# Kernel tuning notes

Hardware: AMD Instinct MI355X
Metric: run time of the kernel (lower is better)

## Reference

```python
import jax, jax.numpy as jnp
import numpy as np

N, E, G = 50000, 200000, 64
F, H, C = 1536, 1024, 80
FUSE = 1024


def setup_inputs() -> dict:
    key = jax.random.key(0)
    ks = jax.random.split(key, 12)
    def lin(k, fan_in, shape):
        return jax.random.normal(k, shape, dtype=jnp.float32) / np.sqrt(fan_in)
    return {
        "global_x": jax.random.normal(ks[0], (G, F), dtype=jnp.float32),
        "x": jax.random.normal(ks[1], (N, F), dtype=jnp.float32),
        "edge_index": jax.random.randint(ks[2], (2, E), 0, N),
        "batch": jnp.sort(jax.random.randint(ks[3], (N,), 0, G)),
        "W1": lin(ks[4], F, (F, H)), "b1": jnp.zeros((H,), jnp.float32),
        "W2": lin(ks[5], H, (H, H)), "b2": jnp.zeros((H,), jnp.float32),
        "fw1": lin(ks[6], F + H, (F + H, FUSE)), "fb1": jnp.zeros((FUSE,), jnp.float32),
        "fw2": lin(ks[7], FUSE, (FUSE, C)), "fb2": jnp.zeros((C,), jnp.float32),
    }


def _gcn_conv(x, src, dst, norm, W, b):
    # x' = D^-1/2 (A+I) D^-1/2 (x W) + b   (PyG GCNConv, add_self_loops=True)
    h = x @ W                                   # [N, H]
    msg = h[src] * norm[:, None]                # [E+N, H] gather + scale
    out = jax.ops.segment_sum(msg, dst, num_segments=N)  # scatter-add
    return out + b


def reference(global_x, x, edge_index, batch, W1, b1, W2, b2, fw1, fb1, fw2, fb2):
    loops = jnp.arange(N)
    src = jnp.concatenate([edge_index[0], loops])  # add self-loops
    dst = jnp.concatenate([edge_index[1], loops])
    deg = jax.ops.segment_sum(jnp.ones(E + N, jnp.float32), dst, num_segments=N)
    dis = jnp.where(deg > 0, jax.lax.rsqrt(jnp.maximum(deg, 1.0)), 0.0)
    norm = dis[src] * dis[dst]                  # symmetric normalization

    h = jax.nn.relu(_gcn_conv(x, src, dst, norm, W1, b1))
    h = jax.nn.relu(_gcn_conv(h, src, dst, norm, W2, b2))

    counts = jax.ops.segment_sum(jnp.ones(N, jnp.float32), batch, num_segments=G)
    pooled = jax.ops.segment_sum(h, batch, num_segments=G) / jnp.maximum(counts, 1.0)[:, None]

    combined = jnp.concatenate([global_x, pooled], axis=1)  # [G, F+H]
    hid = jax.nn.relu(combined @ fw1 + fb1)     # dropout is identity in eval
    return hid @ fw2 + fb2                      # [G, C]
```

## Files before the change

### kernel.cpp

```cpp
#include <hip/hip_runtime.h>
#include <stdint.h>

#define N_NODES 50000
#define N_EDGES 200000
#define N_GRAPH 64
#define F_IN    1536
#define H_DIM   1024
#define C_OUT   80
#define FUSE_D  1024
#define POOL_CHUNK 128
#define MLP1_KC 320
#define SCAN_B  49

typedef unsigned short u16;
typedef short s16x8 __attribute__((ext_vector_type(8)));
typedef float f32x4 __attribute__((ext_vector_type(4)));
typedef unsigned short u16x4 __attribute__((ext_vector_type(4)));
typedef unsigned short u16x8 __attribute__((ext_vector_type(8)));

__device__ __forceinline__ float bf2f(u16 u) {
    union { unsigned int i; float f; } v; v.i = ((unsigned int)u) << 16; return v.f;
}
__device__ __forceinline__ u16 f2bf(float f) {
    union { float f; unsigned int i; } v; v.f = f;
    unsigned int x = v.i;
    unsigned int r = (x + 0x7fffu + ((x >> 16) & 1u)) >> 16;
    return (u16)r;
}

__device__ __forceinline__ void load_lds16(const void* g, void* l) {
    __builtin_amdgcn_global_load_lds(
        (const __attribute__((address_space(1))) void*)g,
        (__attribute__((address_space(3))) void*)l, 16, 0, 0);
}

__global__ void k_deg(const int* __restrict__ dst, int* cnt) {
    int e = blockIdx.x * blockDim.x + threadIdx.x;
    if (e < N_EDGES) atomicAdd(&cnt[dst[e]], 1);
}

__global__ void k_cg(const int* __restrict__ batch, int* cG) {
    int i = blockIdx.x * blockDim.x + threadIdx.x;
    if (i < N_NODES) atomicAdd(&cG[batch[i]], 1);
}

__global__ __launch_bounds__(1024) void k_scan_a(const int* __restrict__ cnt, int* __restrict__ bsum) {
    __shared__ int lds[1024];
    int t = threadIdx.x;
    int i = blockIdx.x * 1024 + t;
    lds[t] = (i < N_NODES) ? cnt[i] : 0;
    __syncthreads();
    for (int off = 512; off > 0; off >>= 1) {
        if (t < off) lds[t] += lds[t + off];
        __syncthreads();
    }
    if (t == 0) bsum[blockIdx.x] = lds[0];
}

__global__ __launch_bounds__(64) void k_scan_b(const int* __restrict__ bsum,
                                               int* __restrict__ boff, int* __restrict__ rowptr) {
    int t = threadIdx.x;
    int v = (t < SCAN_B) ? bsum[t] : 0;
    for (int off = 1; off < 64; off <<= 1) {
        int u = __shfl_up(v, off);
        if (t >= off) v += u;
    }
    if (t < SCAN_B) boff[t] = v - bsum[t];
    if (t == SCAN_B - 1) rowptr[N_NODES] = v;
}

__global__ __launch_bounds__(1024) void k_scan_c(const int* __restrict__ cnt, const int* __restrict__ boff,
                                                 int* __restrict__ rowptr, float* __restrict__ dis) {
    __shared__ int lds[1024];
    int t = threadIdx.x;
    int i = blockIdx.x * 1024 + t;
    int c = (i < N_NODES) ? cnt[i] : 0;
    lds[t] = c;
    __syncthreads();
    for (int off = 1; off < 1024; off <<= 1) {
        int u = (t >= off) ? lds[t - off] : 0;
        __syncthreads();
        lds[t] += u;
        __syncthreads();
    }
    if (i < N_NODES) {
        rowptr[i] = boff[blockIdx.x] + lds[t] - c;
        dis[i] = rsqrtf((float)(c + 1));
    }
}

__global__ void k_fill(const int* __restrict__ src, const int* __restrict__ dst,
                       const int* __restrict__ rowptr, int* cursor, int* col) {
    int e = blockIdx.x * blockDim.x + threadIdx.x;
    if (e < N_EDGES) {
        int d = dst[e];
        int p = atomicAdd(&cursor[d], 1);
        col[rowptr[d] + p] = src[e];
    }
}

__global__ void k_cvt(const float* __restrict__ in, u16* __restrict__ out, long n) {
    long i = (long)blockIdx.x * blockDim.x + threadIdx.x;
    long stride = (long)gridDim.x * blockDim.x;
    for (long v = i * 4; v < n; v += stride * 4) {
        float4 f = *(const float4*)(in + v);
        u16x4 o = { f2bf(f.x), f2bf(f.y), f2bf(f.z), f2bf(f.w) };
        *(u16x4*)(out + v) = o;
    }
}

__global__ void k_trn(const float* __restrict__ W, u16* __restrict__ Wt, int K, int Nn) {
    __shared__ float tle[32][33];
    int n0 = blockIdx.x * 32, k0 = blockIdx.y * 32;
    int tx = threadIdx.x, ty = threadIdx.y;
    for (int i = ty; i < 32; i += 8)
        tle[i][tx] = W[(size_t)(k0 + i) * Nn + n0 + tx];
    __syncthreads();
    for (int i = ty; i < 32; i += 8)
        Wt[(size_t)(n0 + i) * K + k0 + tx] = f2bf(tle[tx][i]);
}

__global__ __launch_bounds__(512) void gemm_bt(const u16* __restrict__ A,
                                               const u16* __restrict__ Bt,
                                               u16* __restrict__ C,
                                               int M, int Nn, int K) {
    __shared__ __attribute__((aligned(16))) u16 ldsA[2 * 2048 * 8];
    __shared__ __attribute__((aligned(16))) u16 ldsB[2 * 2048 * 8];

    int bid = blockIdx.x;
    int swz = (bid & 7) * 98 + (bid >> 3);
    int bN = swz & 3;
    int bM = swz >> 2;

    int tid = threadIdx.x;
    int lane = tid & 63, wave = tid >> 6;
    int wm = wave >> 2, wn = wave & 3;
    int qd = lane >> 4, lo = lane & 15;

    const u16* ga[4];
    const u16* gb[4];
#pragma unroll
    for (int r = 0; r < 4; ++r) {
        int c = r * 512 + tid;
        int row = c >> 3;
        int kc = (c & 7) ^ (row & 7);
        int gr = bM * 256 + row;
        if (gr > M - 1) gr = M - 1;
        ga[r] = A + (size_t)gr * K + kc * 8;
        gb[r] = Bt + (size_t)(bN * 256 + row) * K + kc * 8;
    }

    auto stage = [&](int buf) {
        int base = buf * 16384;
#pragma unroll
        for (int r = 0; r < 4; ++r) {
            load_lds16(ga[r], &ldsA[base + (r * 512 + tid) * 8]);
            ga[r] += 64;
        }
#pragma unroll
        for (int r = 0; r < 4; ++r) {
            load_lds16(gb[r], &ldsB[base + (r * 512 + tid) * 8]);
            gb[r] += 64;
        }
    };

    const int NKT = K >> 6;
    f32x4 acc[8][4] = {};

    stage(0);
    stage(1);

    for (int kt = 0; kt < NKT; ++kt) {
        int cur = kt & 1;
        if (kt < NKT - 1) {
            asm volatile("s_waitcnt vmcnt(8)" ::: "memory");
        } else {
            asm volatile("s_waitcnt vmcnt(0)" ::: "memory");
        }
        __builtin_amdgcn_s_barrier();

        const u16* lA = ldsA + cur * 16384;
        const u16* lB = ldsB + cur * 16384;
#pragma unroll
        for (int ks = 0; ks < 2; ++ks) {
            s16x8 af[8], bfv[4];
            int soff = (((ks << 2) + qd) ^ (lo & 7)) * 8;
#pragma unroll
            for (int mf = 0; mf < 8; ++mf)
                af[mf] = *(const s16x8*)&lA[(wm * 128 + mf * 16 + lo) * 64 + soff];
#pragma unroll
            for (int nf = 0; nf < 4; ++nf)
                bfv[nf] = *(const s16x8*)&lB[(wn * 64 + nf * 16 + lo) * 64 + soff];
            __builtin_amdgcn_s_setprio(1);
#pragma unroll
            for (int mf = 0; mf < 8; ++mf)
#pragma unroll
                for (int nf = 0; nf < 4; ++nf)
                    acc[mf][nf] = __builtin_amdgcn_mfma_f32_16x16x32_bf16(
                        af[mf], bfv[nf], acc[mf][nf], 0, 0, 0);
            __builtin_amdgcn_s_setprio(0);
            __builtin_amdgcn_s_barrier();
        }
        if (kt + 2 < NKT) stage(cur);
    }

#pragma unroll
    for (int mf = 0; mf < 8; ++mf) {
        int rowb = bM * 256 + wm * 128 + mf * 16 + qd * 4;
#pragma unroll
        for (int nf = 0; nf < 4; ++nf) {
            int colI = bN * 256 + wn * 64 + nf * 16 + lo;
            f32x4 a = acc[mf][nf];
#pragma unroll
            for (int reg = 0; reg < 4; ++reg) {
                int row = rowb + reg;
                if (row < M) C[(size_t)row * Nn + colI] = f2bf(a[reg]);
            }
        }
    }
}

__global__ __launch_bounds__(256) void k_agg(const u16* __restrict__ hin, u16* __restrict__ hout,
                                             const int* __restrict__ rowptr, const int* __restrict__ col,
                                             const float* __restrict__ dis, const float* __restrict__ bias) {
    int w = threadIdx.x >> 6, lane = threadIdx.x & 63;
    int i = blockIdx.x * 4 + w;
    float di = dis[i];
    int beg = rowptr[i], end = rowptr[i + 1];
    const u16* hrow = hin + (size_t)i * H_DIM + lane * 16;
    u16x8 v0 = *(const u16x8*)hrow;
    u16x8 v1 = *(const u16x8*)(hrow + 8);
    float w0 = di * di;
    float acc[16];
#pragma unroll
    for (int j = 0; j < 8; j++) { acc[j] = w0 * bf2f(v0[j]); acc[8 + j] = w0 * bf2f(v1[j]); }
    int e = beg;
    for (; e + 2 <= end; e += 2) {
        int s0 = col[e], s1 = col[e + 1];
        float g0 = di * dis[s0], g1 = di * dis[s1];
        const u16* n0 = hin + (size_t)s0 * H_DIM + lane * 16;
        const u16* n1 = hin + (size_t)s1 * H_DIM + lane * 16;
        u16x8 a0 = *(const u16x8*)n0;
        u16x8 a1 = *(const u16x8*)(n0 + 8);
        u16x8 b0 = *(const u16x8*)n1;
        u16x8 b1 = *(const u16x8*)(n1 + 8);
#pragma unroll
        for (int j = 0; j < 8; j++) {
            acc[j]     += g0 * bf2f(a0[j]) + g1 * bf2f(b0[j]);
            acc[8 + j] += g0 * bf2f(a1[j]) + g1 * bf2f(b1[j]);
        }
    }
    if (e < end) {
        int s = col[e];
        float wgt = di * dis[s];
        const u16* nrow = hin + (size_t)s * H_DIM + lane * 16;
        u16x8 u0 = *(const u16x8*)nrow;
        u16x8 u1 = *(const u16x8*)(nrow + 8);
#pragma unroll
        for (int j = 0; j < 8; j++) { acc[j] += wgt * bf2f(u0[j]); acc[8 + j] += wgt * bf2f(u1[j]); }
    }
    const float* bp = bias + lane * 16;
    u16x8 o0, o1;
#pragma unroll
    for (int j = 0; j < 8; j++) {
        o0[j] = f2bf(fmaxf(acc[j] + bp[j], 0.f));
        o1[j] = f2bf(fmaxf(acc[8 + j] + bp[8 + j], 0.f));
    }
    u16* orow = hout + (size_t)i * H_DIM + lane * 16;
    *(u16x8*)orow = o0;
    *(u16x8*)(orow + 8) = o1;
}

__global__ __launch_bounds__(256) void k_pool(const u16* __restrict__ h, const int* __restrict__ batch,
                                              float* __restrict__ pooled) {
    int t = threadIdx.x;
    int n0 = blockIdx.x * POOL_CHUNK;
    int n1 = min(n0 + POOL_CHUNK, N_NODES);
    float a0 = 0.f, a1 = 0.f, a2 = 0.f, a3 = 0.f;
    int curg = batch[n0];
    for (int n = n0; n < n1; ++n) {
        int g = batch[n];
        if (g != curg) {
            float* p = &pooled[(size_t)curg * H_DIM + t * 4];
            atomicAdd(p + 0, a0); atomicAdd(p + 1, a1);
            atomicAdd(p + 2, a2); atomicAdd(p + 3, a3);
            a0 = a1 = a2 = a3 = 0.f;
            curg = g;
        }
        u16x4 v = *(const u16x4*)&h[(size_t)n * H_DIM + t * 4];
        a0 += bf2f(v[0]); a1 += bf2f(v[1]); a2 += bf2f(v[2]); a3 += bf2f(v[3]);
    }
    float* p = &pooled[(size_t)curg * H_DIM + t * 4];
    atomicAdd(p + 0, a0); atomicAdd(p + 1, a1);
    atomicAdd(p + 2, a2); atomicAdd(p + 3, a3);
}

__global__ __launch_bounds__(256) void k_mlp1(const float* __restrict__ gx, const float* __restrict__ pooled,
                                              const int* __restrict__ cG,
                                              const float* __restrict__ fw1, float* __restrict__ hid) {
    __shared__ float comb[4 * MLP1_KC];
    int gq = blockIdx.x, jq = blockIdx.y, kq = blockIdx.z, t = threadIdx.x;
    int kbeg = kq * MLP1_KC;
    for (int idx = t; idx < 4 * MLP1_KC; idx += 256) {
        int gl = idx / MLP1_KC, kk = idx % MLP1_KC;
        int k = kbeg + kk;
        int g = gq * 4 + gl;
        float v;
        if (k < F_IN) v = gx[(size_t)g * F_IN + k];
        else v = pooled[(size_t)g * H_DIM + (k - F_IN)] / (float)max(cG[g], 1);
        comb[idx] = v;
    }
    __syncthreads();
    int j = jq * 256 + t;
    float a0 = 0, a1 = 0, a2 = 0, a3 = 0;
    for (int kk = 0; kk < MLP1_KC; ++kk) {
        float w = fw1[(size_t)(kbeg + kk) * FUSE_D + j];
        a0 += comb[kk] * w;
        a1 += comb[MLP1_KC + kk] * w;
        a2 += comb[2 * MLP1_KC + kk] * w;
        a3 += comb[3 * MLP1_KC + kk] * w;
    }
    atomicAdd(&hid[(size_t)(gq * 4 + 0) * FUSE_D + j], a0);
    atomicAdd(&hid[(size_t)(gq * 4 + 1) * FUSE_D + j], a1);
    atomicAdd(&hid[(size_t)(gq * 4 + 2) * FUSE_D + j], a2);
    atomicAdd(&hid[(size_t)(gq * 4 + 3) * FUSE_D + j], a3);
}

__global__ __launch_bounds__(128) void k_mlp2(const float* __restrict__ hid, const float* __restrict__ fb1,
                                              const float* __restrict__ fw2,
                                              const float* __restrict__ fb2, float* __restrict__ out) {
    __shared__ float hh[FUSE_D];
    int g = blockIdx.x, t = threadIdx.x;
    for (int idx = t; idx < FUSE_D; idx += 128)
        hh[idx] = fmaxf(hid[(size_t)g * FUSE_D + idx] + fb1[idx], 0.f);
    __syncthreads();
    if (t < C_OUT) {
        float acc = fb2[t];
        for (int k = 0; k < FUSE_D; ++k) acc += hh[k] * fw2[k * C_OUT + t];
        out[g * C_OUT + t] = acc;
    }
}

extern "C" void kernel_launch(void* const* d_in, const int* in_sizes, int n_in,
                              void* d_out, int out_size, void* d_ws, size_t ws_size,
                              hipStream_t stream) {
    (void)in_sizes; (void)n_in; (void)out_size;
    const float* gx    = (const float*)d_in[0];
    const float* x     = (const float*)d_in[1];
    const int*   ei    = (const int*)d_in[2];
    const int*   batch = (const int*)d_in[3];
    const float* W1    = (const float*)d_in[4];
    const float* b1    = (const float*)d_in[5];
    const float* W2    = (const float*)d_in[6];
    const float* b2    = (const float*)d_in[7];
    const float* fw1   = (const float*)d_in[8];
    const float* fb1   = (const float*)d_in[9];
    const float* fw2   = (const float*)d_in[10];
    const float* fb2   = (const float*)d_in[11];
    float* out = (float*)d_out;
    const int* src = ei;
    const int* dst = ei + N_EDGES;

    char* ws = (char*)d_ws;
    size_t off = 0;
    auto alloc = [&](size_t bytes) -> char* {
        char* p = ws + off;
        off += (bytes + 255) & ~(size_t)255;
        return p;
    };
    u16*  xb     = (u16*)alloc((size_t)N_NODES * F_IN * 2);
    u16*  h0b    = (u16*)alloc((size_t)N_NODES * H_DIM * 2);
    u16*  h1b    = (u16*)alloc((size_t)N_NODES * H_DIM * 2);
    u16*  W1T    = (u16*)alloc((size_t)H_DIM * F_IN * 2);
    u16*  W2T    = (u16*)alloc((size_t)H_DIM * H_DIM * 2);
    float* dis    = (float*)alloc((size_t)N_NODES * 4);
    int* rowptr   = (int*)alloc((size_t)(N_NODES + 1) * 4);
    int* col      = (int*)alloc((size_t)N_EDGES * 4);
    int* cnt      = (int*)alloc((size_t)N_NODES * 4);
    int* cursor   = (int*)alloc((size_t)N_NODES * 4);
    int* cG       = (int*)alloc(256);
    float* pooled = (float*)alloc((size_t)N_GRAPH * H_DIM * 4);
    float* hid    = (float*)alloc((size_t)N_GRAPH * FUSE_D * 4);
    u16* h2b = xb;
    u16* h3b = h0b;
    int* bsum = col;
    int* boff = col + 64;
    (void)ws_size;

    size_t zbytes = (size_t)((char*)(hid + N_GRAPH * FUSE_D) - (char*)cnt);
    hipMemsetAsync(cnt, 0, zbytes, stream);

    k_deg<<<(N_EDGES + 255) / 256, 256, 0, stream>>>(dst, cnt);
    k_cg<<<(N_NODES + 255) / 256, 256, 0, stream>>>(batch, cG);
    k_scan_a<<<SCAN_B, 1024, 0, stream>>>(cnt, bsum);
    k_scan_b<<<1, 64, 0, stream>>>(bsum, boff, rowptr);
    k_scan_c<<<SCAN_B, 1024, 0, stream>>>(cnt, boff, rowptr, dis);
    k_fill<<<(N_EDGES + 255) / 256, 256, 0, stream>>>(src, dst, rowptr, cursor, col);

    k_cvt<<<4096, 256, 0, stream>>>(x, xb, (long)N_NODES * F_IN);
    k_trn<<<dim3(H_DIM / 32, F_IN / 32), dim3(32, 8), 0, stream>>>(W1, W1T, F_IN, H_DIM);
    k_trn<<<dim3(H_DIM / 32, H_DIM / 32), dim3(32, 8), 0, stream>>>(W2, W2T, H_DIM, H_DIM);

    const int GEMM_BLOCKS = ((N_NODES + 255) / 256) * (H_DIM / 256);

    gemm_bt<<<GEMM_BLOCKS, 512, 0, stream>>>(xb, W1T, h0b, N_NODES, H_DIM, F_IN);
    k_agg<<<N_NODES / 4, 256, 0, stream>>>(h0b, h1b, rowptr, col, dis, b1);
    gemm_bt<<<GEMM_BLOCKS, 512, 0, stream>>>(h1b, W2T, h2b, N_NODES, H_DIM, H_DIM);
    k_agg<<<N_NODES / 4, 256, 0, stream>>>(h2b, h3b, rowptr, col, dis, b2);

    k_pool<<<(N_NODES + POOL_CHUNK - 1) / POOL_CHUNK, 256, 0, stream>>>(h3b, batch, pooled);
    k_mlp1<<<dim3(N_GRAPH / 4, FUSE_D / 256, 8), 256, 0, stream>>>(gx, pooled, cG, fw1, hid);
    k_mlp2<<<N_GRAPH, 128, 0, stream>>>(hid, fb1, fw2, fb2, out);
}
```

Baseline: 1.500 ms.

## Deepen GEMM LDS pipeline to 4 stages with K-tile 32; widen MLP1 graph batching

The bf16 GEMM now uses a K-tile of 32 instead of 64, with four LDS buffers and three tiles prefetched ahead. The swizzle is adapted to 4-chunk rows, and one of the two barriers per iteration is removed. The aim is to hide global-load latency better while keeping the same LDS footprint. The cost is twice as many loop iterations, each doing half the MFMA work, so per-iteration overhead is relatively larger. MLP1 also handles 8 graphs per block instead of 4, which halves the number of fw1 weight reads.

```diff
diff --git a/kernel.cpp b/kernel.cpp
--- a/kernel.cpp
+++ b/kernel.cpp
@@ -10,6 +10,7 @@
 #define FUSE_D  1024
 #define POOL_CHUNK 128
 #define MLP1_KC 320
+#define MLP1_G  8
 #define SCAN_B  49
 
 typedef unsigned short u16;
@@ -124,8 +125,8 @@
                                                const u16* __restrict__ Bt,
                                                u16* __restrict__ C,
                                                int M, int Nn, int K) {
-    __shared__ __attribute__((aligned(16))) u16 ldsA[2 * 2048 * 8];
-    __shared__ __attribute__((aligned(16))) u16 ldsB[2 * 2048 * 8];
+    __shared__ __attribute__((aligned(16))) u16 ldsA[4 * 8192];
+    __shared__ __attribute__((aligned(16))) u16 ldsB[4 * 8192];
 
     int bid = blockIdx.x;
     int swz = (bid & 7) * 98 + (bid >> 3);
@@ -137,13 +138,13 @@
     int wm = wave >> 2, wn = wave & 3;
     int qd = lane >> 4, lo = lane & 15;
 
-    const u16* ga[4];
-    const u16* gb[4];
-#pragma unroll
-    for (int r = 0; r < 4; ++r) {
+    const u16* ga[2];
+    const u16* gb[2];
+#pragma unroll
+    for (int r = 0; r < 2; ++r) {
         int c = r * 512 + tid;
-        int row = c >> 3;
-        int kc = (c & 7) ^ (row & 7);
+        int row = c >> 2;
+        int kc = (c & 3) ^ ((row >> 1) & 3);
         int gr = bM * 256 + row;
         if (gr > M - 1) gr = M - 1;
         ga[r] = A + (size_t)gr * K + kc * 8;
@@ -151,57 +152,58 @@
     }
 
     auto stage = [&](int buf) {
-        int base = buf * 16384;
-#pragma unroll
-        for (int r = 0; r < 4; ++r) {
+        int base = buf * 8192;
+#pragma unroll
+        for (int r = 0; r < 2; ++r)
             load_lds16(ga[r], &ldsA[base + (r * 512 + tid) * 8]);
-            ga[r] += 64;
-        }
-#pragma unroll
-        for (int r = 0; r < 4; ++r) {
+#pragma unroll
+        for (int r = 0; r < 2; ++r)
             load_lds16(gb[r], &ldsB[base + (r * 512 + tid) * 8]);
-            gb[r] += 64;
-        }
+#pragma unroll
+        for (int r = 0; r < 2; ++r) { ga[r] += 32; gb[r] += 32; }
     };
 
-    const int NKT = K >> 6;
+    const int NKT = K >> 5;
     f32x4 acc[8][4] = {};
 
     stage(0);
     stage(1);
+    stage(2);
+
+    const int sl = (qd ^ ((lo >> 1) & 3)) * 8;
 
     for (int kt = 0; kt < NKT; ++kt) {
-        int cur = kt & 1;
-        if (kt < NKT - 1) {
+        int cur = kt & 3;
+        if (kt < NKT - 2) {
             asm volatile("s_waitcnt vmcnt(8)" ::: "memory");
+        } else if (kt == NKT - 2) {
+            asm volatile("s_waitcnt vmcnt(4)" ::: "memory");
         } else {
             asm volatile("s_waitcnt vmcnt(0)" ::: "memory");
         }
         __builtin_amdgcn_s_barrier();
 
-        const u16* lA = ldsA + cur * 16384;
-        const u16* lB = ldsB + cur * 16384;
-#pragma unroll
-        for (int ks = 0; ks < 2; ++ks) {
-            s16x8 af[8], bfv[4];
-            int soff = (((ks << 2) + qd) ^ (lo & 7)) * 8;
-#pragma unroll
-            for (int mf = 0; mf < 8; ++mf)
-                af[mf] = *(const s16x8*)&lA[(wm * 128 + mf * 16 + lo) * 64 + soff];
+        const u16* lA = ldsA + cur * 8192;
+        const u16* lB = ldsB + cur * 8192;
+        s16x8 af[8], bv[4];
+#pragma unroll
+        for (int mf = 0; mf < 8; ++mf)
+            af[mf] = *(const s16x8*)&lA[(wm * 128 + mf * 16 + lo) * 32 + sl];
+#pragma unroll
+        for (int nf = 0; nf < 4; ++nf)
+            bv[nf] = *(const s16x8*)&lB[(wn * 64 + nf * 16 + lo) * 32 + sl];
+        asm volatile("s_waitcnt lgkmcnt(0)" ::: "memory");
+        __builtin_amdgcn_sched_barrier(0);
+        __builtin_amdgcn_s_setprio(1);
+#pragma unroll
+        for (int mf = 0; mf < 8; ++mf)
 #pragma unroll
             for (int nf = 0; nf < 4; ++nf)
-                bfv[nf] = *(const s16x8*)&lB[(wn * 64 + nf * 16 + lo) * 64 + soff];
-            __builtin_amdgcn_s_setprio(1);
-#pragma unroll
-            for (int mf = 0; mf < 8; ++mf)
-#pragma unroll
-                for (int nf = 0; nf < 4; ++nf)
-                    acc[mf][nf] = __builtin_amdgcn_mfma_f32_16x16x32_bf16(
-                        af[mf], bfv[nf], acc[mf][nf], 0, 0, 0);
-            __builtin_amdgcn_s_setprio(0);
-            __builtin_amdgcn_s_barrier();
-        }
-        if (kt + 2 < NKT) stage(cur);
+                acc[mf][nf] = __builtin_amdgcn_mfma_f32_16x16x32_bf16(
+                    af[mf], bv[nf], acc[mf][nf], 0, 0, 0);
+        __builtin_amdgcn_s_setprio(0);
+
+        if (kt + 3 < NKT) stage((kt + 3) & 3);
     }
 
 #pragma unroll
@@ -298,13 +300,13 @@
 __global__ __launch_bounds__(256) void k_mlp1(const float* __restrict__ gx, const float* __restrict__ pooled,
                                               const int* __restrict__ cG,
                                               const float* __restrict__ fw1, float* __restrict__ hid) {
-    __shared__ float comb[4 * MLP1_KC];
+    __shared__ float comb[MLP1_G * MLP1_KC];
     int gq = blockIdx.x, jq = blockIdx.y, kq = blockIdx.z, t = threadIdx.x;
     int kbeg = kq * MLP1_KC;
-    for (int idx = t; idx < 4 * MLP1_KC; idx += 256) {
+    for (int idx = t; idx < MLP1_G * MLP1_KC; idx += 256) {
         int gl = idx / MLP1_KC, kk = idx % MLP1_KC;
         int k = kbeg + kk;
-        int g = gq * 4 + gl;
+        int g = gq * MLP1_G + gl;
         float v;
         if (k < F_IN) v = gx[(size_t)g * F_IN + k];
         else v = pooled[(size_t)g * H_DIM + (k - F_IN)] / (float)max(cG[g], 1);
@@ -312,18 +314,18 @@
     }
     __syncthreads();
     int j = jq * 256 + t;
-    float a0 = 0, a1 = 0, a2 = 0, a3 = 0;
+    float a[MLP1_G];
+#pragma unroll
+    for (int gl = 0; gl < MLP1_G; ++gl) a[gl] = 0.f;
     for (int kk = 0; kk < MLP1_KC; ++kk) {
         float w = fw1[(size_t)(kbeg + kk) * FUSE_D + j];
-        a0 += comb[kk] * w;
-        a1 += comb[MLP1_KC + kk] * w;
-        a2 += comb[2 * MLP1_KC + kk] * w;
-        a3 += comb[3 * MLP1_KC + kk] * w;
-    }
-    atomicAdd(&hid[(size_t)(gq * 4 + 0) * FUSE_D + j], a0);
-    atomicAdd(&hid[(size_t)(gq * 4 + 1) * FUSE_D + j], a1);
-    atomicAdd(&hid[(size_t)(gq * 4 + 2) * FUSE_D + j], a2);
-    atomicAdd(&hid[(size_t)(gq * 4 + 3) * FUSE_D + j], a3);
+#pragma unroll
+        for (int gl = 0; gl < MLP1_G; ++gl)
+            a[gl] += comb[gl * MLP1_KC + kk] * w;
+    }
+#pragma unroll
+    for (int gl = 0; gl < MLP1_G; ++gl)
+        atomicAdd(&hid[(size_t)(gq * MLP1_G + gl) * FUSE_D + j], a[gl]);
 }
 
 __global__ __launch_bounds__(128) void k_mlp2(const float* __restrict__ hid, const float* __restrict__ fb1,
@@ -409,6 +411,6 @@
     k_agg<<<N_NODES / 4, 256, 0, stream>>>(h2b, h3b, rowptr, col, dis, b2);
 
     k_pool<<<(N_NODES + POOL_CHUNK - 1) / POOL_CHUNK, 256, 0, stream>>>(h3b, batch, pooled);
-    k_mlp1<<<dim3(N_GRAPH / 4, FUSE_D / 256, 8), 256, 0, stream>>>(gx, pooled, cG, fw1, hid);
+    k_mlp1<<<dim3(N_GRAPH / MLP1_G, FUSE_D / 256, 8), 256, 0, stream>>>(gx, pooled, cG, fw1, hid);
     k_mlp2<<<N_GRAPH, 128, 0, stream>>>(hid, fb1, fw2, fb2, out);
 }
```

New measurement: 1.500 ms. About the same (+0.0%).
